# Kernel optimization log

Hardware: AMD Instinct MI355X
Metric: run time of the kernel (lower is better)

The kernel has to match this reference:

```python
import jax, jax.numpy as jnp
import numpy as np

N_NODES = 20000
IN_FEAT = 256
OUT_FEAT = 128
N_EDGES = 640000


def setup_inputs() -> dict:
    key = jax.random.key(0)
    k1, k2, k3 = jax.random.split(key, 3)
    x = jax.random.normal(k1, (N_NODES, IN_FEAT), dtype=jnp.float32)
    edge_index = jax.random.randint(k2, (2, N_EDGES), 0, N_NODES, dtype=jnp.int64)
    # Xavier-uniform init for weight, zeros for bias (as in reset_parameters)
    limit = np.sqrt(6.0 / (IN_FEAT + OUT_FEAT)).astype(np.float32)
    weight = jax.random.uniform(k3, (IN_FEAT, OUT_FEAT), dtype=jnp.float32,
                                minval=-limit, maxval=limit)
    bias = jnp.zeros((OUT_FEAT,), dtype=jnp.float32)
    return {"x": x, "edge_index": edge_index, "weight": weight, "bias": bias}


def reference(x, edge_index, weight, bias):
    # [N, in] @ [in, out] -> [N, out]
    h = jnp.matmul(x, weight)
    row, col = edge_index[0], edge_index[1]
    # gather source-node features along edges, scatter-add into destination
    out = jax.ops.segment_sum(h[col], row, num_segments=x.shape[0])  # [N, out]
    return jax.nn.relu(out + bias)
```

## Files before the change

kernel.cpp:

```cpp
#include <hip/hip_runtime.h>

#define IN_FEAT 256
#define OUT_FEAT 128
#define CAP 64

typedef __bf16 bf16x8 __attribute__((ext_vector_type(8)));
typedef float f32x4 __attribute__((ext_vector_type(4)));

__device__ __forceinline__ float bf_lo(unsigned u) { return __builtin_bit_cast(float, u << 16); }
__device__ __forceinline__ float bf_hi(unsigned u) { return __builtin_bit_cast(float, u & 0xffff0000u); }

__global__ __launch_bounds__(256) void build_kernel(
        const float* __restrict__ w, unsigned short* __restrict__ wt,
        const int* __restrict__ edges, int* __restrict__ cnt,
        int* __restrict__ slots, int* __restrict__ ovf_cnt,
        int2* __restrict__ ovf, int n_edges, int n_nodes) {
    const int b = blockIdx.x;
    if (b < 16) {
        int t = b * 256 + threadIdx.x;
        int n  = t >> 5;
        int k0 = (t & 31) * 8;
        union { unsigned short s[8]; uint4 u; } p;
        #pragma unroll
        for (int i = 0; i < 8; ++i) {
            __bf16 v = (__bf16)w[(k0 + i) * OUT_FEAT + n];
            p.s[i] = __builtin_bit_cast(unsigned short, v);
        }
        *reinterpret_cast<uint4*>(&wt[n * IN_FEAT + k0]) = p.u;
        return;
    }
    const int t = (b - 16) * 256 + threadIdx.x;
    const int ne4 = n_edges >> 2;
    if (t < ne4) {
        int4 r = *reinterpret_cast<const int4*>(&edges[t * 4]);
        int4 c = *reinterpret_cast<const int4*>(&edges[n_edges + t * 4]);
        #pragma unroll
        for (int j = 0; j < 4; ++j) {
            int rr = (&r.x)[j], cc = (&c.x)[j];
            if ((unsigned)rr < (unsigned)n_nodes && (unsigned)cc < (unsigned)n_nodes) {
                int pos = atomicAdd(&cnt[rr], 1);
                if (pos < CAP) slots[rr * CAP + pos] = cc;
                else           ovf[atomicAdd(ovf_cnt, 1)] = make_int2(rr, cc);
            }
        }
    }
    if (b == 16 && threadIdx.x == 0) {
        for (int e = ne4 * 4; e < n_edges; ++e) {
            int rr = edges[e], cc = edges[n_edges + e];
            if ((unsigned)rr < (unsigned)n_nodes && (unsigned)cc < (unsigned)n_nodes) {
                int pos = atomicAdd(&cnt[rr], 1);
                if (pos < CAP) slots[rr * CAP + pos] = cc;
                else           ovf[atomicAdd(ovf_cnt, 1)] = make_int2(rr, cc);
            }
        }
    }
}

__global__ __launch_bounds__(256) void gemm_kernel(
        const float* __restrict__ x, const unsigned short* __restrict__ wt,
        unsigned short* __restrict__ h, int n_nodes) {
    const int tid = threadIdx.x;
    const int rowtile = blockIdx.x >> 1;
    const int nfbase  = (blockIdx.x & 1) * 4;
    const int wid = tid >> 6;
    const int l   = tid & 63;
    const int lr  = l & 15;
    const int lg  = l >> 4;
    const int row = rowtile * 64 + wid * 16 + lr;
    const int rowc = row < n_nodes ? row : n_nodes - 1;
    const float* xrow = x + (long long)rowc * IN_FEAT;

    f32x4 acc[4];
    #pragma unroll
    for (int i = 0; i < 4; ++i) acc[i] = (f32x4){0.f, 0.f, 0.f, 0.f};

    #pragma unroll 2
    for (int kk = 0; kk < 8; ++kk) {
        const int k0 = kk * 32 + lg * 8;
        float4 xa = *reinterpret_cast<const float4*>(xrow + k0);
        float4 xb = *reinterpret_cast<const float4*>(xrow + k0 + 4);
        bf16x8 a;
        a[0] = (__bf16)xa.x; a[1] = (__bf16)xa.y;
        a[2] = (__bf16)xa.z; a[3] = (__bf16)xa.w;
        a[4] = (__bf16)xb.x; a[5] = (__bf16)xb.y;
        a[6] = (__bf16)xb.z; a[7] = (__bf16)xb.w;
        #pragma unroll
        for (int nf = 0; nf < 4; ++nf) {
            uint4 braw = *reinterpret_cast<const uint4*>(
                &wt[((nfbase + nf) * 16 + lr) * IN_FEAT + k0]);
            bf16x8 bfr = __builtin_bit_cast(bf16x8, braw);
            acc[nf] = __builtin_amdgcn_mfma_f32_16x16x32_bf16(bfr, a, acc[nf], 0, 0, 0);
        }
    }

    if (row < n_nodes) {
        unsigned short* hrow = h + (long long)row * OUT_FEAT;
        #pragma unroll
        for (int nf = 0; nf < 4; ++nf) {
            union { unsigned short s[4]; uint2 u; } p;
            #pragma unroll
            for (int r = 0; r < 4; ++r) {
                __bf16 v = (__bf16)acc[nf][r];
                p.s[r] = __builtin_bit_cast(unsigned short, v);
            }
            *reinterpret_cast<uint2*>(&hrow[(nfbase + nf) * 16 + lg * 4]) = p.u;
        }
    }
}

__global__ __launch_bounds__(256) void agg_kernel(
        const unsigned short* __restrict__ h, const int* __restrict__ cnt,
        const int* __restrict__ slots, const int* __restrict__ ovf_cnt,
        const int2* __restrict__ ovf, const float* __restrict__ bias,
        float* __restrict__ out, int n_nodes) {
    const int node = blockIdx.x * 4 + (threadIdx.x >> 6);
    if (node >= n_nodes) return;
    const int l = threadIdx.x & 63;
    const int g = l >> 4;
    const int fl = l & 15;

    int deg = cnt[node];
    if (deg > CAP) deg = CAP;
    const int* sl = slots + node * CAP;
    const unsigned short* hb = h + fl * 8;

    float a0 = 0.f, a1 = 0.f, a2 = 0.f, a3 = 0.f;
    float a4 = 0.f, a5 = 0.f, a6 = 0.f, a7 = 0.f;

    int e = g;
    for (; e + 4 < deg; e += 8) {
        int c0 = sl[e];
        int c1 = sl[e + 4];
        uint4 r0 = *reinterpret_cast<const uint4*>(hb + (long long)c0 * OUT_FEAT);
        uint4 r1 = *reinterpret_cast<const uint4*>(hb + (long long)c1 * OUT_FEAT);
        a0 += bf_lo(r0.x); a1 += bf_hi(r0.x);
        a2 += bf_lo(r0.y); a3 += bf_hi(r0.y);
        a4 += bf_lo(r0.z); a5 += bf_hi(r0.z);
        a6 += bf_lo(r0.w); a7 += bf_hi(r0.w);
        a0 += bf_lo(r1.x); a1 += bf_hi(r1.x);
        a2 += bf_lo(r1.y); a3 += bf_hi(r1.y);
        a4 += bf_lo(r1.z); a5 += bf_hi(r1.z);
        a6 += bf_lo(r1.w); a7 += bf_hi(r1.w);
    }
    if (e < deg) {
        int c0 = sl[e];
        uint4 r0 = *reinterpret_cast<const uint4*>(hb + (long long)c0 * OUT_FEAT);
        a0 += bf_lo(r0.x); a1 += bf_hi(r0.x);
        a2 += bf_lo(r0.y); a3 += bf_hi(r0.y);
        a4 += bf_lo(r0.z); a5 += bf_hi(r0.z);
        a6 += bf_lo(r0.w); a7 += bf_hi(r0.w);
    }

    int no = *ovf_cnt;
    if (no > 0 && g == 0) {
        for (int i = 0; i < no; ++i) {
            int2 rc = ovf[i];
            if (rc.x == node) {
                uint4 r0 = *reinterpret_cast<const uint4*>(hb + (long long)rc.y * OUT_FEAT);
                a0 += bf_lo(r0.x); a1 += bf_hi(r0.x);
                a2 += bf_lo(r0.y); a3 += bf_hi(r0.y);
                a4 += bf_lo(r0.z); a5 += bf_hi(r0.z);
                a6 += bf_lo(r0.w); a7 += bf_hi(r0.w);
            }
        }
    }

    #pragma unroll
    for (int d = 16; d <= 32; d <<= 1) {
        a0 += __shfl_xor(a0, d, 64); a1 += __shfl_xor(a1, d, 64);
        a2 += __shfl_xor(a2, d, 64); a3 += __shfl_xor(a3, d, 64);
        a4 += __shfl_xor(a4, d, 64); a5 += __shfl_xor(a5, d, 64);
        a6 += __shfl_xor(a6, d, 64); a7 += __shfl_xor(a7, d, 64);
    }

    if (g == 0) {
        const float* bp = bias + fl * 8;
        float4 b0 = *reinterpret_cast<const float4*>(bp);
        float4 b1 = *reinterpret_cast<const float4*>(bp + 4);
        float4 o0, o1;
        o0.x = fmaxf(a0 + b0.x, 0.f); o0.y = fmaxf(a1 + b0.y, 0.f);
        o0.z = fmaxf(a2 + b0.z, 0.f); o0.w = fmaxf(a3 + b0.w, 0.f);
        o1.x = fmaxf(a4 + b1.x, 0.f); o1.y = fmaxf(a5 + b1.y, 0.f);
        o1.z = fmaxf(a6 + b1.z, 0.f); o1.w = fmaxf(a7 + b1.w, 0.f);
        float* op = out + (long long)node * OUT_FEAT + fl * 8;
        *reinterpret_cast<float4*>(op) = o0;
        *reinterpret_cast<float4*>(op + 4) = o1;
    }
}

extern "C" void kernel_launch(void* const* d_in, const int* in_sizes, int n_in,
                              void* d_out, int out_size, void* d_ws, size_t ws_size,
                              hipStream_t stream) {
    const float* x      = (const float*)d_in[0];
    const int*   edges  = (const int*)d_in[1];
    const float* weight = (const float*)d_in[2];
    const float* bias   = (const float*)d_in[3];
    float* out = (float*)d_out;

    const int n_nodes = in_sizes[0] / IN_FEAT;
    const int n_edges = in_sizes[1] / 2;

    char* ws = (char*)d_ws;
    size_t off = 0;
    unsigned short* h = (unsigned short*)(ws + off);
    off += (size_t)n_nodes * OUT_FEAT * 2;
    unsigned short* wt = (unsigned short*)(ws + off);
    off += (size_t)IN_FEAT * OUT_FEAT * 2;
    int* cnt = (int*)(ws + off);
    int* ovf_cnt = cnt + n_nodes;
    off += (((size_t)n_nodes + 1) * 4 + 15) & ~(size_t)15;
    int* slots = (int*)(ws + off);
    off += (size_t)n_nodes * CAP * 4;
    int2* ovf = (int2*)(ws + off);
    off += (size_t)n_edges * 8;

    hipMemsetAsync(cnt, 0, ((size_t)n_nodes + 1) * 4, stream);

    int fill_blocks = (n_edges / 4 + 255) / 256;
    build_kernel<<<16 + fill_blocks, 256, 0, stream>>>(
        weight, wt, edges, cnt, slots, ovf_cnt, ovf, n_edges, n_nodes);

    int rowtiles = (n_nodes + 63) / 64;
    gemm_kernel<<<rowtiles * 2, 256, 0, stream>>>(x, wt, h, n_nodes);

    agg_kernel<<<(n_nodes + 3) / 4, 256, 0, stream>>>(
        h, cnt, slots, ovf_cnt, ovf, bias, out, n_nodes);
}
```

Before: 148.2 us.

## Fuse edge bucketing into GEMM launch and fold counter zeroing into prep

Replaces the hipMemsetAsync with a kernel that zeroes the per-node counters and also converts the weight to bf16, removing one launch/API call. The edge-bucketing fill work moves out of the weight-prep kernel into the GEMM kernel as extra blocks, so the compute-bound MFMA work and the atomic-heavy scatter can run concurrently in one launch. This reshapes the cross-stage schedule: weight prep no longer waits behind edge filling, at the cost of a larger heterogeneous grid whose block scheduling order now matters.

```diff
diff --git a/kernel.cpp b/kernel.cpp
--- a/kernel.cpp
+++ b/kernel.cpp
@@ -10,11 +10,9 @@
 __device__ __forceinline__ float bf_lo(unsigned u) { return __builtin_bit_cast(float, u << 16); }
 __device__ __forceinline__ float bf_hi(unsigned u) { return __builtin_bit_cast(float, u & 0xffff0000u); }
 
-__global__ __launch_bounds__(256) void build_kernel(
+__global__ __launch_bounds__(256) void prep_kernel(
         const float* __restrict__ w, unsigned short* __restrict__ wt,
-        const int* __restrict__ edges, int* __restrict__ cnt,
-        int* __restrict__ slots, int* __restrict__ ovf_cnt,
-        int2* __restrict__ ovf, int n_edges, int n_nodes) {
+        int* __restrict__ cnt, int n_cnt) {
     const int b = blockIdx.x;
     if (b < 16) {
         int t = b * 256 + threadIdx.x;
@@ -27,9 +25,72 @@
             p.s[i] = __builtin_bit_cast(unsigned short, v);
         }
         *reinterpret_cast<uint4*>(&wt[n * IN_FEAT + k0]) = p.u;
+    } else {
+        int i = (b - 16) * 256 + threadIdx.x;
+        if (i < n_cnt) cnt[i] = 0;
+    }
+}
+
+__global__ __launch_bounds__(256) void gemm_fill_kernel(
+        const float* __restrict__ x, const unsigned short* __restrict__ wt,
+        unsigned short* __restrict__ h,
+        const int* __restrict__ edges, int* __restrict__ cnt,
+        int* __restrict__ slots, int* __restrict__ ovf_cnt,
+        int2* __restrict__ ovf,
+        int n_nodes, int n_edges, int gemm_blocks) {
+    if ((int)blockIdx.x < gemm_blocks) {
+        const int tid = threadIdx.x;
+        const int rowtile = blockIdx.x >> 1;
+        const int nfbase  = (blockIdx.x & 1) * 4;
+        const int wid = tid >> 6;
+        const int l   = tid & 63;
+        const int lr  = l & 15;
+        const int lg  = l >> 4;
+        const int row = rowtile * 64 + wid * 16 + lr;
+        const int rowc = row < n_nodes ? row : n_nodes - 1;
+        const float* xrow = x + (long long)rowc * IN_FEAT;
+
+        f32x4 acc[4];
+        #pragma unroll
+        for (int i = 0; i < 4; ++i) acc[i] = (f32x4){0.f, 0.f, 0.f, 0.f};
+
+        #pragma unroll 2
+        for (int kk = 0; kk < 8; ++kk) {
+            const int k0 = kk * 32 + lg * 8;
+            float4 xa = *reinterpret_cast<const float4*>(xrow + k0);
+            float4 xb = *reinterpret_cast<const float4*>(xrow + k0 + 4);
+            bf16x8 a;
+            a[0] = (__bf16)xa.x; a[1] = (__bf16)xa.y;
+            a[2] = (__bf16)xa.z; a[3] = (__bf16)xa.w;
+            a[4] = (__bf16)xb.x; a[5] = (__bf16)xb.y;
+            a[6] = (__bf16)xb.z; a[7] = (__bf16)xb.w;
+            #pragma unroll
+            for (int nf = 0; nf < 4; ++nf) {
+                uint4 braw = *reinterpret_cast<const uint4*>(
+                    &wt[((nfbase + nf) * 16 + lr) * IN_FEAT + k0]);
+                bf16x8 bfr = __builtin_bit_cast(bf16x8, braw);
+                acc[nf] = __builtin_amdgcn_mfma_f32_16x16x32_bf16(bfr, a, acc[nf], 0, 0, 0);
+            }
+        }
+
+        if (row < n_nodes) {
+            unsigned short* hrow = h + (long long)row * OUT_FEAT;
+            #pragma unroll
+            for (int nf = 0; nf < 4; ++nf) {
+                union { unsigned short s[4]; uint2 u; } p;
+                #pragma unroll
+                for (int r = 0; r < 4; ++r) {
+                    __bf16 v = (__bf16)acc[nf][r];
+                    p.s[r] = __builtin_bit_cast(unsigned short, v);
+                }
+                *reinterpret_cast<uint2*>(&hrow[(nfbase + nf) * 16 + lg * 4]) = p.u;
+            }
+        }
         return;
     }
-    const int t = (b - 16) * 256 + threadIdx.x;
+
+    const int fb = blockIdx.x - gemm_blocks;
+    const int t = fb * 256 + threadIdx.x;
     const int ne4 = n_edges >> 2;
     if (t < ne4) {
         int4 r = *reinterpret_cast<const int4*>(&edges[t * 4]);
@@ -44,7 +105,7 @@
             }
         }
     }
-    if (b == 16 && threadIdx.x == 0) {
+    if (fb == 0 && threadIdx.x == 0) {
         for (int e = ne4 * 4; e < n_edges; ++e) {
             int rr = edges[e], cc = edges[n_edges + e];
             if ((unsigned)rr < (unsigned)n_nodes && (unsigned)cc < (unsigned)n_nodes) {
@@ -52,58 +113,6 @@
                 if (pos < CAP) slots[rr * CAP + pos] = cc;
                 else           ovf[atomicAdd(ovf_cnt, 1)] = make_int2(rr, cc);
             }
-        }
-    }
-}
-
-__global__ __launch_bounds__(256) void gemm_kernel(
-        const float* __restrict__ x, const unsigned short* __restrict__ wt,
-        unsigned short* __restrict__ h, int n_nodes) {
-    const int tid = threadIdx.x;
-    const int rowtile = blockIdx.x >> 1;
-    const int nfbase  = (blockIdx.x & 1) * 4;
-    const int wid = tid >> 6;
-    const int l   = tid & 63;
-    const int lr  = l & 15;
-    const int lg  = l >> 4;
-    const int row = rowtile * 64 + wid * 16 + lr;
-    const int rowc = row < n_nodes ? row : n_nodes - 1;
-    const float* xrow = x + (long long)rowc * IN_FEAT;
-
-    f32x4 acc[4];
-    #pragma unroll
-    for (int i = 0; i < 4; ++i) acc[i] = (f32x4){0.f, 0.f, 0.f, 0.f};
-
-    #pragma unroll 2
-    for (int kk = 0; kk < 8; ++kk) {
-        const int k0 = kk * 32 + lg * 8;
-        float4 xa = *reinterpret_cast<const float4*>(xrow + k0);
-        float4 xb = *reinterpret_cast<const float4*>(xrow + k0 + 4);
-        bf16x8 a;
-        a[0] = (__bf16)xa.x; a[1] = (__bf16)xa.y;
-        a[2] = (__bf16)xa.z; a[3] = (__bf16)xa.w;
-        a[4] = (__bf16)xb.x; a[5] = (__bf16)xb.y;
-        a[6] = (__bf16)xb.z; a[7] = (__bf16)xb.w;
-        #pragma unroll
-        for (int nf = 0; nf < 4; ++nf) {
-            uint4 braw = *reinterpret_cast<const uint4*>(
-                &wt[((nfbase + nf) * 16 + lr) * IN_FEAT + k0]);
-            bf16x8 bfr = __builtin_bit_cast(bf16x8, braw);
-            acc[nf] = __builtin_amdgcn_mfma_f32_16x16x32_bf16(bfr, a, acc[nf], 0, 0, 0);
-        }
-    }
-
-    if (row < n_nodes) {
-        unsigned short* hrow = h + (long long)row * OUT_FEAT;
-        #pragma unroll
-        for (int nf = 0; nf < 4; ++nf) {
-            union { unsigned short s[4]; uint2 u; } p;
-            #pragma unroll
-            for (int r = 0; r < 4; ++r) {
-                __bf16 v = (__bf16)acc[nf][r];
-                p.s[r] = __builtin_bit_cast(unsigned short, v);
-            }
-            *reinterpret_cast<uint2*>(&hrow[(nfbase + nf) * 16 + lg * 4]) = p.u;
         }
     }
 }
@@ -214,14 +223,13 @@
     int2* ovf = (int2*)(ws + off);
     off += (size_t)n_edges * 8;
 
-    hipMemsetAsync(cnt, 0, ((size_t)n_nodes + 1) * 4, stream);
-
-    int fill_blocks = (n_edges / 4 + 255) / 256;
-    build_kernel<<<16 + fill_blocks, 256, 0, stream>>>(
-        weight, wt, edges, cnt, slots, ovf_cnt, ovf, n_edges, n_nodes);
-
-    int rowtiles = (n_nodes + 63) / 64;
-    gemm_kernel<<<rowtiles * 2, 256, 0, stream>>>(x, wt, h, n_nodes);
+    int zero_blocks = (n_nodes + 1 + 255) / 256;
+    prep_kernel<<<16 + zero_blocks, 256, 0, stream>>>(weight, wt, cnt, n_nodes + 1);
+
+    int gb = ((n_nodes + 63) / 64) * 2;
+    int fb = (n_edges / 4 + 255) / 256;
+    gemm_fill_kernel<<<gb + fb, 256, 0, stream>>>(
+        x, wt, h, edges, cnt, slots, ovf_cnt, ovf, n_nodes, n_edges, gb);
 
     agg_kernel<<<(n_nodes + 3) / 4, 256, 0, stream>>>(
         h, cnt, slots, ovf_cnt, ovf, bias, out, n_nodes);
```

Result: faster. 130.3 us (-12.1%).
